# Performance work log

Measured on AMD Instinct MI355X. Metric: run time of the kernel, lower is better.

## Reference

```python
import jax, jax.numpy as jnp
import numpy as np

N_NODES = 50000
N_EDGES = 800000
N_GRAPHS = 8
BN_EPS = 1e-5


def setup_inputs() -> dict:
    key = jax.random.key(0)
    ks = iter(jax.random.split(key, 40))
    d = {}
    d["x"] = jax.random.normal(next(ks), (N_NODES, 3), dtype=jnp.float32)
    d["edge_index"] = jax.random.randint(next(ks), (2, N_EDGES), 0, N_NODES, dtype=jnp.int32)
    d["batch"] = jnp.sort(jax.random.randint(next(ks), (N_NODES,), 0, N_GRAPHS, dtype=jnp.int32))
    conv_in = [3, 64, 128]  # dense concat widths feeding each GCN layer
    for i, cin in enumerate(conv_in):
        d[f"W{i}"] = jax.random.normal(next(ks), (cin, 64), dtype=jnp.float32) * (1.0 / np.sqrt(cin))
        d[f"b{i}"] = jax.random.normal(next(ks), (64,), dtype=jnp.float32) * 0.05
        d[f"g{i}"] = jax.random.uniform(next(ks), (64,), dtype=jnp.float32) + 0.5
        d[f"beta{i}"] = jax.random.normal(next(ks), (64,), dtype=jnp.float32) * 0.05
        d[f"rm{i}"] = jax.random.normal(next(ks), (64,), dtype=jnp.float32) * 0.05
        d[f"rv{i}"] = jax.random.uniform(next(ks), (64,), dtype=jnp.float32) + 0.5
    def lin(k, i, o):
        return (jax.random.normal(k, (i, o), dtype=jnp.float32) * (1.0 / np.sqrt(i)),)
    d["enc_w0"], = lin(next(ks), 256, 128); d["enc_b0"] = jax.random.normal(next(ks), (128,), jnp.float32) * 0.05
    d["enc_w1"], = lin(next(ks), 128, 64); d["enc_b1"] = jax.random.normal(next(ks), (64,), jnp.float32) * 0.05
    d["dec_w0"], = lin(next(ks), 64, 32); d["dec_b0"] = jax.random.normal(next(ks), (32,), jnp.float32) * 0.05
    d["dec_w1"], = lin(next(ks), 32, 1); d["dec_b1"] = jax.random.normal(next(ks), (1,), jnp.float32) * 0.05
    return d


def reference(x, edge_index, batch,
              W0, b0, g0, beta0, rm0, rv0,
              W1, b1, g1, beta1, rm1, rv1,
              W2, b2, g2, beta2, rm2, rv2,
              enc_w0, enc_b0, enc_w1, enc_b1,
              dec_w0, dec_b0, dec_w1, dec_b1):
    N = x.shape[0]
    loops = jnp.arange(N, dtype=edge_index.dtype)
    src = jnp.concatenate([edge_index[0], loops])  # GCNConv adds self loops
    dst = jnp.concatenate([edge_index[1], loops])
    deg = jax.ops.segment_sum(jnp.ones_like(src, dtype=x.dtype), dst, num_segments=N)
    dinv = jnp.where(deg > 0, jax.lax.rsqrt(deg), 0.0)
    coef = (dinv[src] * dinv[dst])[:, None]  # symmetric normalization per edge

    def conv_bn_relu(h, W, b, g, beta, rm, rv):
        hw = h @ W                                    # [N, 64]
        out = jax.ops.segment_sum(hw[src] * coef, dst, num_segments=N) + b
        out = (out - rm) * (g * jax.lax.rsqrt(rv + BN_EPS)) + beta  # BN eval mode
        return jax.nn.relu(out)

    params = [(W0, b0, g0, beta0, rm0, rv0),
              (W1, b1, g1, beta1, rm1, rv1),
              (W2, b2, g2, beta2, rm2, rv2)]
    prev = []
    h = x
    for p in params:  # dense connectivity: concat all previous concat-outputs
        h = conv_bn_relu(h, *p)
        h = jnp.concatenate(prev + [h], axis=1)
        prev.append(h)

    e = jax.nn.relu(jax.nn.relu(h @ enc_w0 + enc_b0) @ enc_w1 + enc_b1)  # [N, 64]
    counts = jax.ops.segment_sum(jnp.ones((N,), x.dtype), batch, num_segments=N_GRAPHS)
    gfeat = jax.ops.segment_sum(e, batch, num_segments=N_GRAPHS) / jnp.maximum(counts, 1.0)[:, None]
    out = jax.nn.relu(gfeat @ dec_w0 + dec_b0) @ dec_w1 + dec_b1  # [G, 1]
    return out[:, 0]  # torch.squeeze(output, 1) since num_classes == 1
```

## Files before the change

### kernel.cpp

```cpp
#include <hip/hip_runtime.h>
#include <hip/hip_fp16.h>

#define NN 50000
#define NE 800000
#define NG 8
#define BN_EPS 1e-5f
#define NBLK ((NN + 255) / 256)
#define NPART 8
#define HLD 192

typedef __attribute__((ext_vector_type(8))) short bf16x8;
typedef __attribute__((ext_vector_type(4))) float f32x4;

static __device__ __forceinline__ unsigned short f2bf(float f) {
    unsigned int u = __float_as_uint(f);
    unsigned int r = (u + 0x7FFFu + ((u >> 16) & 1u)) >> 16;
    return (unsigned short)r;
}
static __device__ __forceinline__ float bf2f(unsigned short h) {
    return __uint_as_float((unsigned int)h << 16);
}


__global__ __launch_bounds__(256) void count_deg(const int* __restrict__ dst,
                                                 int* __restrict__ degi) {
    int e = blockIdx.x * 256 + threadIdx.x;
    if (e < NE) atomicAdd(&degi[dst[e]], 1);
}

__global__ __launch_bounds__(256) void scan_partial(const int* __restrict__ degi,
                                                    const float* __restrict__ x,
                                                    int* __restrict__ rowptr,
                                                    int* __restrict__ bsum,
                                                    float* __restrict__ dinv,
                                                    float* __restrict__ xs) {
    __shared__ int sh[256];
    const int tid = threadIdx.x;
    const int i = blockIdx.x * 256 + tid;
    int v = (i < NN) ? degi[i] : 0;
    if (i < NN) {
        float di = rsqrtf((float)(v + 1));
        dinv[i] = di;
        xs[i * 3 + 0] = x[i * 3 + 0] * di;
        xs[i * 3 + 1] = x[i * 3 + 1] * di;
        xs[i * 3 + 2] = x[i * 3 + 2] * di;
    }
    sh[tid] = v;
    __syncthreads();
#pragma unroll
    for (int off = 1; off < 256; off <<= 1) {
        int t = (tid >= off) ? sh[tid - off] : 0;
        __syncthreads();
        sh[tid] += t;
        __syncthreads();
    }
    if (i < NN) rowptr[i] = sh[tid] - v;
    if (tid == 255) bsum[blockIdx.x] = sh[255];
}

__global__ __launch_bounds__(256) void scan_bsums(int* __restrict__ bsum) {
    __shared__ int sh[256];
    const int tid = threadIdx.x;
    int v = (tid < NBLK) ? bsum[tid] : 0;
    sh[tid] = v;
    __syncthreads();
#pragma unroll
    for (int off = 1; off < 256; off <<= 1) {
        int t = (tid >= off) ? sh[tid - off] : 0;
        __syncthreads();
        sh[tid] += t;
        __syncthreads();
    }
    if (tid < NBLK) bsum[tid] = sh[tid] - v;
}

__global__ __launch_bounds__(256) void scan_finalize(const int* __restrict__ bsum,
                                                     int* __restrict__ rowptr,
                                                     int* __restrict__ cursor) {
    const int i = blockIdx.x * 256 + threadIdx.x;
    if (i < NN) {
        int r = rowptr[i] + bsum[blockIdx.x];
        rowptr[i] = r;
        cursor[i] = r;
    }
    if (i == 0) rowptr[NN] = NE;
}

__global__ __launch_bounds__(256) void fill_csr(const int* __restrict__ src,
                                                const int* __restrict__ dst,
                                                int* __restrict__ cursor,
                                                unsigned short* __restrict__ esrc16) {
    int e = blockIdx.x * 256 + threadIdx.x;
    if (e < NE) {
        int s = src[e], d = dst[e];
        int p = atomicAdd(&cursor[d], 1);
        esrc16[p] = (unsigned short)s;
    }
}


static __device__ __forceinline__ void pack_one(const float* W, int NOUT, int li,
                                                float v_override, bool use_override,
                                                unsigned short* ph, unsigned short* pl) {
    int j = li & 7;
    int lane = (li >> 3) & 63;
    int rest = li >> 9;
    int NF = NOUT >> 4;
    int f = rest % NF, ks = rest / NF;
    int k = ks * 32 + (lane >> 4) * 8 + j;
    int col = f * 16 + (lane & 15);
    float v = use_override ? v_override : W[k * NOUT + col];
    unsigned short hi = f2bf(v);
    ph[li] = hi;
    pl[li] = f2bf(v - bf2f(hi));
}

__global__ __launch_bounds__(256) void pack_all(
        const float* __restrict__ W1, const float* __restrict__ W2,
        const float* __restrict__ We0, const float* __restrict__ We1,
        unsigned short* __restrict__ Wp1h, unsigned short* __restrict__ Wp1l,
        unsigned short* __restrict__ Wp2h, unsigned short* __restrict__ Wp2l,
        unsigned short* __restrict__ We0h, unsigned short* __restrict__ We0l,
        unsigned short* __restrict__ We1h, unsigned short* __restrict__ We1l) {
    int idx = blockIdx.x * 256 + threadIdx.x;
    if (idx < 4096) {
        pack_one(W1, 64, idx, 0.f, false, Wp1h, Wp1l);
    } else if (idx < 12288) {
        pack_one(W2, 64, idx - 4096, 0.f, false, Wp2h, Wp2l);
    } else if (idx < 36864) {
        int li = idx - 12288;
        int j = li & 7;
        int lane = (li >> 3) & 63;
        int rest = li >> 9;
        int f = rest % 8, ks = rest / 8;
        int k = ks * 32 + (lane >> 4) * 8 + j;
        int col = f * 16 + (lane & 15);
        float v = (k < 64) ? (We0[k * 128 + col] + We0[(k + 64) * 128 + col])
                           : We0[(k + 64) * 128 + col];
        pack_one(nullptr, 128, li, v, true, We0h, We0l);
    } else if (idx < 45056) {
        pack_one(We1, 64, idx - 36864, 0.f, false, We1h, We1l);
    }
}


template<int K>
__global__ __launch_bounds__(256, 2) void mfma_tab(
        const unsigned short* __restrict__ Ahi,
        const unsigned short* __restrict__ Alo, int lda,
        const unsigned short* __restrict__ Bph,
        const unsigned short* __restrict__ Bpl,
        const float* __restrict__ dinv,
        __half* __restrict__ outH) {
    constexpr int KS = K / 32;
    const int wave = threadIdx.x >> 6;
    const int lane = threadIdx.x & 63;
    const int rbase = blockIdx.x * 64 + wave * 16;
    int arow = rbase + (lane & 15);
    if (arow >= NN) arow = NN - 1;
    const int kbase = (lane >> 4) * 8;

    bf16x8 bh[KS][4], bl[KS][4];
#pragma unroll
    for (int ks = 0; ks < KS; ks++)
#pragma unroll
        for (int f = 0; f < 4; f++) {
            bh[ks][f] = *reinterpret_cast<const bf16x8*>(Bph + (size_t)((ks * 4 + f) * 64 + lane) * 8);
            bl[ks][f] = *reinterpret_cast<const bf16x8*>(Bpl + (size_t)((ks * 4 + f) * 64 + lane) * 8);
        }

    const unsigned short* pa_hi = Ahi + (size_t)arow * lda + kbase;
    const unsigned short* pa_lo = Alo + (size_t)arow * lda + kbase;
    bf16x8 ah[KS], al[KS];
#pragma unroll
    for (int ks = 0; ks < KS; ks++) {
        ah[ks] = *reinterpret_cast<const bf16x8*>(pa_hi + ks * 32);
        al[ks] = *reinterpret_cast<const bf16x8*>(pa_lo + ks * 32);
    }

    f32x4 acc[4];
#pragma unroll
    for (int f = 0; f < 4; f++) acc[f] = (f32x4){0.f, 0.f, 0.f, 0.f};

#pragma unroll
    for (int ks = 0; ks < KS; ks++)
#pragma unroll
        for (int f = 0; f < 4; f++) {
            acc[f] = __builtin_amdgcn_mfma_f32_16x16x32_bf16(ah[ks], bh[ks][f], acc[f], 0, 0, 0);
            acc[f] = __builtin_amdgcn_mfma_f32_16x16x32_bf16(ah[ks], bl[ks][f], acc[f], 0, 0, 0);
            acc[f] = __builtin_amdgcn_mfma_f32_16x16x32_bf16(al[ks], bh[ks][f], acc[f], 0, 0, 0);
        }

    const int drow0 = rbase + (lane >> 4) * 4;
    const int dcol = lane & 15;
#pragma unroll
    for (int f = 0; f < 4; f++) {
#pragma unroll
        for (int r = 0; r < 4; r++) {
            int row = drow0 + r;
            if (row < NN)
                outH[(size_t)row * 64 + f * 16 + dcol] = __float2half(acc[f][r] * dinv[row]);
        }
    }
}


__global__ __launch_bounds__(256, 2) void enc_fused(
        const unsigned short* __restrict__ Hhi,
        const unsigned short* __restrict__ Hlo,
        const unsigned short* __restrict__ We0h, const unsigned short* __restrict__ We0l,
        const float* __restrict__ b0,
        const unsigned short* __restrict__ We1h, const unsigned short* __restrict__ We1l,
        const float* __restrict__ b1,
        const int* __restrict__ batch,
        float* __restrict__ gfeat_part) {
    __shared__ float ldsT[4][16][133];
    __shared__ float poolw[4][64];
    __shared__ float pool[NG][64];
    const int tid = threadIdx.x;
    const int wave = tid >> 6;
    const int lane = tid & 63;
    const int rbase = blockIdx.x * 64 + wave * 16;

    int arow = rbase + (lane & 15);
    if (arow >= NN) arow = NN - 1;
    const int kbase = (lane >> 4) * 8;
    f32x4 acc[8];
#pragma unroll
    for (int f = 0; f < 8; f++) acc[f] = (f32x4){0.f, 0.f, 0.f, 0.f};

    const unsigned short* pa_hi = Hhi + (size_t)arow * HLD + kbase;
    const unsigned short* pa_lo = Hlo + (size_t)arow * HLD + kbase;

    bf16x8 cbh[8], cbl[8], nbh[8], nbl[8];
#pragma unroll
    for (int f = 0; f < 8; f++) {
        cbh[f] = *reinterpret_cast<const bf16x8*>(We0h + (size_t)(f * 64 + lane) * 8);
        cbl[f] = *reinterpret_cast<const bf16x8*>(We0l + (size_t)(f * 64 + lane) * 8);
    }
#pragma unroll
    for (int ks = 0; ks < 6; ks++) {
        if (ks < 5) {
#pragma unroll
            for (int f = 0; f < 8; f++) {
                nbh[f] = *reinterpret_cast<const bf16x8*>(We0h + (size_t)(((ks + 1) * 8 + f) * 64 + lane) * 8);
                nbl[f] = *reinterpret_cast<const bf16x8*>(We0l + (size_t)(((ks + 1) * 8 + f) * 64 + lane) * 8);
            }
        }
        bf16x8 ah = *reinterpret_cast<const bf16x8*>(pa_hi + ks * 32);
        bf16x8 al = *reinterpret_cast<const bf16x8*>(pa_lo + ks * 32);
#pragma unroll
        for (int f = 0; f < 8; f++) {
            acc[f] = __builtin_amdgcn_mfma_f32_16x16x32_bf16(ah, cbh[f], acc[f], 0, 0, 0);
            acc[f] = __builtin_amdgcn_mfma_f32_16x16x32_bf16(ah, cbl[f], acc[f], 0, 0, 0);
            acc[f] = __builtin_amdgcn_mfma_f32_16x16x32_bf16(al, cbh[f], acc[f], 0, 0, 0);
        }
        if (ks < 5) {
#pragma unroll
            for (int f = 0; f < 8; f++) { cbh[f] = nbh[f]; cbl[f] = nbl[f]; }
        }
    }

    const int lrow0 = (lane >> 4) * 4;
    const int dcol = lane & 15;
#pragma unroll
    for (int f = 0; f < 8; f++) {
#pragma unroll
        for (int r = 0; r < 4; r++) {
            float v = fmaxf(acc[f][r] + b0[f * 16 + dcol], 0.0f);
            ldsT[wave][lrow0 + r][f * 16 + dcol] = v;
        }
    }
    __syncthreads();

    bf16x8 wbh[4][4], wbl[4][4];
#pragma unroll
    for (int ks = 0; ks < 4; ks++)
#pragma unroll
        for (int f = 0; f < 4; f++) {
            wbh[ks][f] = *reinterpret_cast<const bf16x8*>(We1h + (size_t)((ks * 4 + f) * 64 + lane) * 8);
            wbl[ks][f] = *reinterpret_cast<const bf16x8*>(We1l + (size_t)((ks * 4 + f) * 64 + lane) * 8);
        }

    f32x4 acc2[4];
#pragma unroll
    for (int f = 0; f < 4; f++) acc2[f] = (f32x4){0.f, 0.f, 0.f, 0.f};

    const int trow = lane & 15;
#pragma unroll
    for (int ks = 0; ks < 4; ks++) {
        bf16x8 ah, al;
#pragma unroll
        for (int j = 0; j < 8; j++) {
            float tv = ldsT[wave][trow][ks * 32 + (lane >> 4) * 8 + j];
            unsigned short hi = f2bf(tv);
            ah[j] = (short)hi;
            al[j] = (short)f2bf(tv - bf2f(hi));
        }
#pragma unroll
        for (int f = 0; f < 4; f++) {
            acc2[f] = __builtin_amdgcn_mfma_f32_16x16x32_bf16(ah, wbh[ks][f], acc2[f], 0, 0, 0);
            acc2[f] = __builtin_amdgcn_mfma_f32_16x16x32_bf16(ah, wbl[ks][f], acc2[f], 0, 0, 0);
            acc2[f] = __builtin_amdgcn_mfma_f32_16x16x32_bf16(al, wbh[ks][f], acc2[f], 0, 0, 0);
        }
    }

    float vout[4][4];
#pragma unroll
    for (int f = 0; f < 4; f++)
#pragma unroll
        for (int r = 0; r < 4; r++) {
            int row = rbase + lrow0 + r;
            vout[f][r] = (row < NN) ? fmaxf(acc2[f][r] + b1[f * 16 + dcol], 0.0f) : 0.0f;
        }

    const int blk_row0 = blockIdx.x * 64;
    const int blk_rowN = min(blk_row0 + 63, NN - 1);
    const int g0 = batch[blk_row0];
    const int p = blockIdx.x & (NPART - 1);

    if (g0 == batch[blk_rowN]) {
#pragma unroll
        for (int f = 0; f < 4; f++) {
            float s = (vout[f][0] + vout[f][1]) + (vout[f][2] + vout[f][3]);
            s += __shfl_xor(s, 16, 64);
            s += __shfl_xor(s, 32, 64);
            if ((lane >> 4) == 0) poolw[wave][f * 16 + dcol] = s;
        }
        __syncthreads();
        if (tid < 64) {
            float s = (poolw[0][tid] + poolw[1][tid]) + (poolw[2][tid] + poolw[3][tid]);
            atomicAdd(&gfeat_part[(p * NG + g0) * 64 + tid], s);
        }
    } else {
        for (int i = tid; i < NG * 64; i += 256) ((float*)pool)[i] = 0.0f;
        __syncthreads();
#pragma unroll
        for (int r = 0; r < 4; r++) {
            int row = rbase + lrow0 + r;
            if (row < NN) {
                int g = batch[row];
#pragma unroll
                for (int f = 0; f < 4; f++)
                    atomicAdd(&pool[g][f * 16 + dcol], vout[f][r]);
            }
        }
        __syncthreads();
        for (int i = tid; i < NG * 64; i += 256) {
            float s = ((float*)pool)[i];
            if (s != 0.0f) atomicAdd(&gfeat_part[p * NG * 64 + i], s);
        }
    }
}


__global__ __launch_bounds__(256) void agg_x3(
        const float* __restrict__ xs,
        const int* __restrict__ rowptr,
        const unsigned short* __restrict__ esrc16,
        const float* __restrict__ dinv,
        float* __restrict__ ax) {
    const int i = blockIdx.x * 256 + threadIdx.x;
    if (i >= NN) return;
    float a0 = xs[i * 3 + 0];
    float a1 = xs[i * 3 + 1];
    float a2 = xs[i * 3 + 2];
    const int beg = rowptr[i], end = rowptr[i + 1];
    int e = beg;
    for (; e + 3 < end; e += 4) {
        int s0 = esrc16[e], s1 = esrc16[e + 1], s2 = esrc16[e + 2], s3 = esrc16[e + 3];
        a0 += xs[s0 * 3 + 0] + xs[s1 * 3 + 0] + xs[s2 * 3 + 0] + xs[s3 * 3 + 0];
        a1 += xs[s0 * 3 + 1] + xs[s1 * 3 + 1] + xs[s2 * 3 + 1] + xs[s3 * 3 + 1];
        a2 += xs[s0 * 3 + 2] + xs[s1 * 3 + 2] + xs[s2 * 3 + 2] + xs[s3 * 3 + 2];
    }
    for (; e < end; e++) {
        int s = esrc16[e];
        a0 += xs[s * 3 + 0];
        a1 += xs[s * 3 + 1];
        a2 += xs[s * 3 + 2];
    }
    const float di = dinv[i];
    ax[i * 3 + 0] = a0 * di;
    ax[i * 3 + 1] = a1 * di;
    ax[i * 3 + 2] = a2 * di;
}


__global__ __launch_bounds__(256) void l0_bn_relu(
        const float* __restrict__ ax, const float* __restrict__ W0,
        const float* __restrict__ b, const float* __restrict__ g,
        const float* __restrict__ beta, const float* __restrict__ rm,
        const float* __restrict__ rv,
        unsigned short* __restrict__ Hhi, unsigned short* __restrict__ Hlo) {
    const int t = blockIdx.x * 256 + threadIdx.x;
    const int row = t >> 6;
    const int ch = t & 63;
    if (row >= NN) return;
    float a0 = ax[row * 3 + 0], a1 = ax[row * 3 + 1], a2 = ax[row * 3 + 2];
    float v = a0 * W0[0 * 64 + ch] + a1 * W0[1 * 64 + ch] + a2 * W0[2 * 64 + ch] + b[ch];
    float sc = g[ch] * rsqrtf(rv[ch] + BN_EPS);
    v = (v - rm[ch]) * sc + beta[ch];
    v = fmaxf(v, 0.0f);
    unsigned short hi = f2bf(v);
    Hhi[(size_t)row * HLD + ch] = hi;
    Hlo[(size_t)row * HLD + ch] = f2bf(v - bf2f(hi));
}


__global__ __launch_bounds__(256) void gather_bn_relu(
        const __half2* __restrict__ tab2,
        const int* __restrict__ rowptr,
        const unsigned short* __restrict__ esrc16,
        const float* __restrict__ dinv,
        const float* __restrict__ b, const float* __restrict__ g,
        const float* __restrict__ beta, const float* __restrict__ rm,
        const float* __restrict__ rv,
        unsigned short* __restrict__ Hhi, unsigned short* __restrict__ Hlo, int cbase) {
    const int wid = (blockIdx.x * 256 + threadIdx.x) >> 6;
    const int lane = threadIdx.x & 63;
    const int c2 = lane & 31;
    const int grp = lane >> 5;
    if (wid >= NN) return;
    const int beg = rowptr[wid], end = rowptr[wid + 1];
    float a0 = 0.0f, a1 = 0.0f;
    int e = beg + grp;
    for (; e + 6 < end; e += 8) {
        int s0 = esrc16[e], s1 = esrc16[e + 2], s2 = esrc16[e + 4], s3 = esrc16[e + 6];
        float2 f0 = __half22float2(tab2[(size_t)s0 * 32 + c2]);
        float2 f1 = __half22float2(tab2[(size_t)s1 * 32 + c2]);
        float2 f2 = __half22float2(tab2[(size_t)s2 * 32 + c2]);
        float2 f3 = __half22float2(tab2[(size_t)s3 * 32 + c2]);
        a0 += (f0.x + f1.x) + (f2.x + f3.x);
        a1 += (f0.y + f1.y) + (f2.y + f3.y);
    }
    for (; e < end; e += 2) {
        float2 f = __half22float2(tab2[(size_t)esrc16[e] * 32 + c2]);
        a0 += f.x;
        a1 += f.y;
    }
    a0 += __shfl_xor(a0, 32, 64);
    a1 += __shfl_xor(a1, 32, 64);
    float2 fs = __half22float2(tab2[(size_t)wid * 32 + c2]);
    a0 += fs.x;
    a1 += fs.y;
    const float di = dinv[wid];
    a0 *= di;
    a1 *= di;
    const int ch0 = 2 * c2, ch1 = 2 * c2 + 1;
    float v0 = (a0 + b[ch0] - rm[ch0]) * (g[ch0] * rsqrtf(rv[ch0] + BN_EPS)) + beta[ch0];
    float v1 = (a1 + b[ch1] - rm[ch1]) * (g[ch1] * rsqrtf(rv[ch1] + BN_EPS)) + beta[ch1];
    v0 = fmaxf(v0, 0.0f);
    v1 = fmaxf(v1, 0.0f);
    if (grp == 0) {
        unsigned short h0 = f2bf(v0), h1 = f2bf(v1);
        unsigned short l0 = f2bf(v0 - bf2f(h0)), l1 = f2bf(v1 - bf2f(h1));
        size_t o = (size_t)wid * HLD + cbase + ch0;
        *reinterpret_cast<unsigned int*>(&Hhi[o]) = (unsigned int)h0 | ((unsigned int)h1 << 16);
        *reinterpret_cast<unsigned int*>(&Hlo[o]) = (unsigned int)l0 | ((unsigned int)l1 << 16);
    }
}


__global__ __launch_bounds__(256) void dec_kernel(
        const float* __restrict__ gfeat_part, const int* __restrict__ batch,
        const float* __restrict__ w0, const float* __restrict__ b0,
        const float* __restrict__ w1, const float* __restrict__ b1,
        float* __restrict__ out) {
    __shared__ float mg[NG][64];
    __shared__ float mc[NG];
    __shared__ float t1[NG][32];
    const int tid = threadIdx.x;
    for (int idx = tid; idx < NG * 64; idx += 256) {
        float s = 0.0f;
#pragma unroll
        for (int p = 0; p < NPART; p++) s += gfeat_part[p * NG * 64 + idx];
        mg[idx >> 6][idx & 63] = s;
    }
    if (tid < NG) {
        int lo = 0, hi = NN;
        while (lo < hi) { int m = (lo + hi) >> 1; if (batch[m] < tid) lo = m + 1; else hi = m; }
        int s0 = lo;
        lo = 0; hi = NN;
        while (lo < hi) { int m = (lo + hi) >> 1; if (batch[m] < tid + 1) lo = m + 1; else hi = m; }
        mc[tid] = (float)(lo - s0);
    }
    __syncthreads();
    const int g = tid >> 5, c = tid & 31;
    float inv = 1.0f / fmaxf(mc[g], 1.0f);
    float acc = b0[c];
    for (int k = 0; k < 64; k++)
        acc = fmaf(mg[g][k] * inv, w0[k * 32 + c], acc);
    t1[g][c] = fmaxf(acc, 0.0f);
    __syncthreads();
    if (tid < NG) {
        float o = b1[0];
        for (int c2 = 0; c2 < 32; c2++) o = fmaf(t1[tid][c2], w1[c2], o);
        out[tid] = o;
    }
}


extern "C" void kernel_launch(void* const* d_in, const int* in_sizes, int n_in,
                              void* d_out, int out_size, void* d_ws, size_t ws_size,
                              hipStream_t stream) {
    const float* x      = (const float*)d_in[0];
    const int*   ei     = (const int*)d_in[1];
    const int*   batch  = (const int*)d_in[2];
    const float* W0     = (const float*)d_in[3];
    const float* b0     = (const float*)d_in[4];
    const float* g0     = (const float*)d_in[5];
    const float* beta0  = (const float*)d_in[6];
    const float* rm0    = (const float*)d_in[7];
    const float* rv0    = (const float*)d_in[8];
    const float* W1     = (const float*)d_in[9];
    const float* b1     = (const float*)d_in[10];
    const float* g1     = (const float*)d_in[11];
    const float* beta1  = (const float*)d_in[12];
    const float* rm1    = (const float*)d_in[13];
    const float* rv1    = (const float*)d_in[14];
    const float* W2     = (const float*)d_in[15];
    const float* b2     = (const float*)d_in[16];
    const float* g2     = (const float*)d_in[17];
    const float* beta2  = (const float*)d_in[18];
    const float* rm2    = (const float*)d_in[19];
    const float* rv2    = (const float*)d_in[20];
    const float* enc_w0 = (const float*)d_in[21];
    const float* enc_b0 = (const float*)d_in[22];
    const float* enc_w1 = (const float*)d_in[23];
    const float* enc_b1 = (const float*)d_in[24];
    const float* dec_w0 = (const float*)d_in[25];
    const float* dec_b0 = (const float*)d_in[26];
    const float* dec_w1 = (const float*)d_in[27];
    const float* dec_b1 = (const float*)d_in[28];

    const int* esrc = ei;
    const int* edst = ei + NE;

    char* wsb = (char*)d_ws;
    unsigned short* Hhi = (unsigned short*)wsb;
    unsigned short* Hlo = Hhi + (size_t)NN * HLD;
    int*   degi   = (int*)(Hlo + (size_t)NN * HLD);
    int*   rowptr = degi + NN;
    int*   cursor = rowptr + NN + 1;
    unsigned short* esrc16 = (unsigned short*)(cursor + NN);
    __half* tabh  = (__half*)(esrc16 + NE);
    float* dinv   = (float*)(tabh + (size_t)NN * 64);
    float* xs     = dinv + NN;
    float* ax     = xs + (size_t)NN * 3;
    float* gfeat_part = ax + (size_t)NN * 3;
    int*   bsum   = (int*)(gfeat_part + NPART * NG * 64);
    unsigned short* wp = (unsigned short*)(bsum + NBLK);
    unsigned short* Wp1h = wp;              unsigned short* Wp1l = Wp1h + 64 * 64;
    unsigned short* Wp2h = Wp1l + 64 * 64;  unsigned short* Wp2l = Wp2h + 128 * 64;
    unsigned short* We0h = Wp2l + 128 * 64; unsigned short* We0l = We0h + 192 * 128;
    unsigned short* We1h = We0l + 192 * 128;unsigned short* We1l = We1h + 128 * 64;

    hipMemsetAsync(gfeat_part, 0, NPART * NG * 64 * sizeof(float), stream);
    hipMemsetAsync(degi, 0, NN * sizeof(int), stream);

    count_deg<<<(NE + 255) / 256, 256, 0, stream>>>(edst, degi);
    scan_partial<<<NBLK, 256, 0, stream>>>(degi, x, rowptr, bsum, dinv, xs);
    scan_bsums<<<1, 256, 0, stream>>>(bsum);
    scan_finalize<<<NBLK, 256, 0, stream>>>(bsum, rowptr, cursor);
    fill_csr<<<(NE + 255) / 256, 256, 0, stream>>>(esrc, edst, cursor, esrc16);

    pack_all<<<(45056 + 255) / 256, 256, 0, stream>>>(W1, W2, enc_w0, enc_w1,
                                                      Wp1h, Wp1l, Wp2h, Wp2l,
                                                      We0h, We0l, We1h, We1l);

    const int GRID_MFMA = (NN + 63) / 64;
    const int GRID_64   = (NN * 64 + 255) / 256;

    agg_x3<<<NBLK, 256, 0, stream>>>(xs, rowptr, esrc16, dinv, ax);
    l0_bn_relu<<<GRID_64, 256, 0, stream>>>(ax, W0, b0, g0, beta0, rm0, rv0, Hhi, Hlo);

    mfma_tab<64><<<GRID_MFMA, 256, 0, stream>>>(Hhi, Hlo, HLD, Wp1h, Wp1l, dinv, tabh);
    gather_bn_relu<<<GRID_64, 256, 0, stream>>>((const __half2*)tabh, rowptr, esrc16, dinv,
                                                b1, g1, beta1, rm1, rv1, Hhi, Hlo, 64);

    mfma_tab<128><<<GRID_MFMA, 256, 0, stream>>>(Hhi, Hlo, HLD, Wp2h, Wp2l, dinv, tabh);
    gather_bn_relu<<<GRID_64, 256, 0, stream>>>((const __half2*)tabh, rowptr, esrc16, dinv,
                                                b2, g2, beta2, rm2, rv2, Hhi, Hlo, 128);

    enc_fused<<<GRID_MFMA, 256, 0, stream>>>(Hhi, Hlo, We0h, We0l, enc_b0,
                                             We1h, We1l, enc_b1, batch, gfeat_part);

    dec_kernel<<<1, 256, 0, stream>>>(gfeat_part, batch, dec_w0, dec_b0, dec_w1, dec_b1, (float*)d_out);
}
```

Before: 244.2 us.

## Split half-precision gather table into two 32-channel halves for cache locality

The MFMA output table is re-laid out as two planar halves of 32 channels each. Each gather pass now runs twice, once per half, with 16 lanes per edge and 4 edges in flight per wavefront. The aim is to shrink the randomly gathered table footprint per pass (about 3.2 MB) so it fits better in L2, at the cost of reading the CSR indices twice and doubling the gather launches. Degree counting also loads destinations as int4, and the gfeat_part memset is folded into pack_all.

```diff
diff --git a/kernel.cpp b/kernel.cpp
--- a/kernel.cpp
+++ b/kernel.cpp
@@ -22,10 +22,16 @@
 }
 
 
-__global__ __launch_bounds__(256) void count_deg(const int* __restrict__ dst,
+__global__ __launch_bounds__(256) void count_deg(const int4* __restrict__ dst4,
                                                  int* __restrict__ degi) {
-    int e = blockIdx.x * 256 + threadIdx.x;
-    if (e < NE) atomicAdd(&degi[dst[e]], 1);
+    int t = blockIdx.x * 256 + threadIdx.x;
+    if (t < NE / 4) {
+        int4 d = dst4[t];
+        atomicAdd(&degi[d.x], 1);
+        atomicAdd(&degi[d.y], 1);
+        atomicAdd(&degi[d.z], 1);
+        atomicAdd(&degi[d.w], 1);
+    }
 }
 
 __global__ __launch_bounds__(256) void scan_partial(const int* __restrict__ degi,
@@ -121,8 +127,10 @@
         unsigned short* __restrict__ Wp1h, unsigned short* __restrict__ Wp1l,
         unsigned short* __restrict__ Wp2h, unsigned short* __restrict__ Wp2l,
         unsigned short* __restrict__ We0h, unsigned short* __restrict__ We0l,
-        unsigned short* __restrict__ We1h, unsigned short* __restrict__ We1l) {
+        unsigned short* __restrict__ We1h, unsigned short* __restrict__ We1l,
+        float* __restrict__ gfeat_part) {
     int idx = blockIdx.x * 256 + threadIdx.x;
+    if (idx < NPART * NG * 64) gfeat_part[idx] = 0.0f;
     if (idx < 4096) {
         pack_one(W1, 64, idx, 0.f, false, Wp1h, Wp1l);
     } else if (idx < 12288) {
@@ -199,7 +207,8 @@
         for (int r = 0; r < 4; r++) {
             int row = drow0 + r;
             if (row < NN)
-                outH[(size_t)row * 64 + f * 16 + dcol] = __float2half(acc[f][r] * dinv[row]);
+                outH[(size_t)(f >> 1) * (NN * 32) + (size_t)row * 32 + (f & 1) * 16 + dcol]
+                    = __float2half(acc[f][r] * dinv[row]);
         }
     }
 }
@@ -407,7 +416,7 @@
 }
 
 
-__global__ __launch_bounds__(256) void gather_bn_relu(
+__global__ __launch_bounds__(256) void gather_bn_relu_h(
         const __half2* __restrict__ tab2,
         const int* __restrict__ rowptr,
         const unsigned short* __restrict__ esrc16,
@@ -415,38 +424,41 @@
         const float* __restrict__ b, const float* __restrict__ g,
         const float* __restrict__ beta, const float* __restrict__ rm,
         const float* __restrict__ rv,
-        unsigned short* __restrict__ Hhi, unsigned short* __restrict__ Hlo, int cbase) {
+        unsigned short* __restrict__ Hhi, unsigned short* __restrict__ Hlo,
+        int cbase, int choff) {
     const int wid = (blockIdx.x * 256 + threadIdx.x) >> 6;
     const int lane = threadIdx.x & 63;
-    const int c2 = lane & 31;
-    const int grp = lane >> 5;
+    const int c2 = lane & 15;
+    const int grp = lane >> 4;
     if (wid >= NN) return;
     const int beg = rowptr[wid], end = rowptr[wid + 1];
     float a0 = 0.0f, a1 = 0.0f;
     int e = beg + grp;
-    for (; e + 6 < end; e += 8) {
-        int s0 = esrc16[e], s1 = esrc16[e + 2], s2 = esrc16[e + 4], s3 = esrc16[e + 6];
-        float2 f0 = __half22float2(tab2[(size_t)s0 * 32 + c2]);
-        float2 f1 = __half22float2(tab2[(size_t)s1 * 32 + c2]);
-        float2 f2 = __half22float2(tab2[(size_t)s2 * 32 + c2]);
-        float2 f3 = __half22float2(tab2[(size_t)s3 * 32 + c2]);
+    for (; e + 12 < end; e += 16) {
+        int s0 = esrc16[e], s1 = esrc16[e + 4], s2 = esrc16[e + 8], s3 = esrc16[e + 12];
+        float2 f0 = __half22float2(tab2[(size_t)s0 * 16 + c2]);
+        float2 f1 = __half22float2(tab2[(size_t)s1 * 16 + c2]);
+        float2 f2 = __half22float2(tab2[(size_t)s2 * 16 + c2]);
+        float2 f3 = __half22float2(tab2[(size_t)s3 * 16 + c2]);
         a0 += (f0.x + f1.x) + (f2.x + f3.x);
         a1 += (f0.y + f1.y) + (f2.y + f3.y);
     }
-    for (; e < end; e += 2) {
-        float2 f = __half22float2(tab2[(size_t)esrc16[e] * 32 + c2]);
+    for (; e < end; e += 4) {
+        float2 f = __half22float2(tab2[(size_t)esrc16[e] * 16 + c2]);
         a0 += f.x;
         a1 += f.y;
     }
+    a0 += __shfl_xor(a0, 16, 64);
     a0 += __shfl_xor(a0, 32, 64);
+    a1 += __shfl_xor(a1, 16, 64);
     a1 += __shfl_xor(a1, 32, 64);
-    float2 fs = __half22float2(tab2[(size_t)wid * 32 + c2]);
+    float2 fs = __half22float2(tab2[(size_t)wid * 16 + c2]);
     a0 += fs.x;
     a1 += fs.y;
     const float di = dinv[wid];
     a0 *= di;
     a1 *= di;
-    const int ch0 = 2 * c2, ch1 = 2 * c2 + 1;
+    const int ch0 = choff + 2 * c2, ch1 = ch0 + 1;
     float v0 = (a0 + b[ch0] - rm[ch0]) * (g[ch0] * rsqrtf(rv[ch0] + BN_EPS)) + beta[ch0];
     float v1 = (a1 + b[ch1] - rm[ch1]) * (g[ch1] * rsqrtf(rv[ch1] + BN_EPS)) + beta[ch1];
     v0 = fmaxf(v0, 0.0f);
@@ -555,10 +567,9 @@
     unsigned short* We0h = Wp2l + 128 * 64; unsigned short* We0l = We0h + 192 * 128;
     unsigned short* We1h = We0l + 192 * 128;unsigned short* We1l = We1h + 128 * 64;
 
-    hipMemsetAsync(gfeat_part, 0, NPART * NG * 64 * sizeof(float), stream);
     hipMemsetAsync(degi, 0, NN * sizeof(int), stream);
 
-    count_deg<<<(NE + 255) / 256, 256, 0, stream>>>(edst, degi);
+    count_deg<<<(NE / 4 + 255) / 256, 256, 0, stream>>>((const int4*)edst, degi);
     scan_partial<<<NBLK, 256, 0, stream>>>(degi, x, rowptr, bsum, dinv, xs);
     scan_bsums<<<1, 256, 0, stream>>>(bsum);
     scan_finalize<<<NBLK, 256, 0, stream>>>(bsum, rowptr, cursor);
@@ -566,21 +577,27 @@
 
     pack_all<<<(45056 + 255) / 256, 256, 0, stream>>>(W1, W2, enc_w0, enc_w1,
                                                       Wp1h, Wp1l, Wp2h, Wp2l,
-                                                      We0h, We0l, We1h, We1l);
+                                                      We0h, We0l, We1h, We1l, gfeat_part);
 
     const int GRID_MFMA = (NN + 63) / 64;
     const int GRID_64   = (NN * 64 + 255) / 256;
+    const __half2* tab0 = (const __half2*)tabh;
+    const __half2* tab1 = (const __half2*)(tabh + (size_t)NN * 32);
 
     agg_x3<<<NBLK, 256, 0, stream>>>(xs, rowptr, esrc16, dinv, ax);
     l0_bn_relu<<<GRID_64, 256, 0, stream>>>(ax, W0, b0, g0, beta0, rm0, rv0, Hhi, Hlo);
 
     mfma_tab<64><<<GRID_MFMA, 256, 0, stream>>>(Hhi, Hlo, HLD, Wp1h, Wp1l, dinv, tabh);
-    gather_bn_relu<<<GRID_64, 256, 0, stream>>>((const __half2*)tabh, rowptr, esrc16, dinv,
-                                                b1, g1, beta1, rm1, rv1, Hhi, Hlo, 64);
+    gather_bn_relu_h<<<GRID_64, 256, 0, stream>>>(tab0, rowptr, esrc16, dinv,
+                                                  b1, g1, beta1, rm1, rv1, Hhi, Hlo, 64, 0);
+    gather_bn_relu_h<<<GRID_64, 256, 0, stream>>>(tab1, rowptr, esrc16, dinv,
+                                                  b1, g1, beta1, rm1, rv1, Hhi, Hlo, 64, 32);
 
     mfma_tab<128><<<GRID_MFMA, 256, 0, stream>>>(Hhi, Hlo, HLD, Wp2h, Wp2l, dinv, tabh);
-    gather_bn_relu<<<GRID_64, 256, 0, stream>>>((const __half2*)tabh, rowptr, esrc16, dinv,
-                                                b2, g2, beta2, rm2, rv2, Hhi, Hlo, 128);
+    gather_bn_relu_h<<<GRID_64, 256, 0, stream>>>(tab0, rowptr, esrc16, dinv,
+                                                  b2, g2, beta2, rm2, rv2, Hhi, Hlo, 128, 0);
+    gather_bn_relu_h<<<GRID_64, 256, 0, stream>>>(tab1, rowptr, esrc16, dinv,
+                                                  b2, g2, beta2, rm2, rv2, Hhi, Hlo, 128, 32);
 
     enc_fused<<<GRID_MFMA, 256, 0, stream>>>(Hhi, Hlo, We0h, We0l, enc_b0,
                                              We1h, We1l, enc_b1, batch, gfeat_part);
```

New measurement: 272.7 us. +11.7%, slower.
